# Kernel tuning notes

Measured on AMD Instinct MI355X. Metric: run time of the kernel, lower is better.

## Reference

```python
import jax, jax.numpy as jnp
import numpy as np

DIM = 128
NUM_HEADS = 8


def setup_inputs() -> dict:
    key = jax.random.key(0)
    ks = jax.random.split(key, 5)
    B, L, C = 4, 16384, DIM
    x = jax.random.normal(ks[0], (B, L, C), dtype=jnp.float32)
    # Linear params (stored as (in, out) so y = x @ W + b)
    w_qkv = jax.random.normal(ks[1], (C, 3 * C), dtype=jnp.float32) * (C ** -0.5)
    b_qkv = jax.random.normal(ks[2], (3 * C,), dtype=jnp.float32) * 0.02
    w_proj = jax.random.normal(ks[3], (C, C), dtype=jnp.float32) * (C ** -0.5)
    b_proj = jax.random.normal(ks[4], (C,), dtype=jnp.float32) * 0.02
    return {"x": x, "w_qkv": w_qkv, "b_qkv": b_qkv, "w_proj": w_proj, "b_proj": b_proj}


def reference(x, w_qkv, b_qkv, w_proj, b_proj):
    B, L, C = x.shape
    H = NUM_HEADS
    hd = C // H
    scale = C ** -0.5  # note: torch code scales by dim**-0.5, not head_dim**-0.5

    qkv = x @ w_qkv + b_qkv                      # (B, L, 3C)
    q, k, v = jnp.split(qkv, 3, axis=-1)         # each (B, L, C)

    def to_heads(t):
        return t.reshape(B, L, H, hd).transpose(0, 2, 1, 3)  # (B, H, L, hd)

    q, k, v = to_heads(q), to_heads(k), to_heads(v)

    # Per-token outer product over head_dim: (B, H, L, hd, hd)
    attn = (q * scale)[..., :, None] * k[..., None, :]
    attn = jax.nn.softmax(attn, axis=-1)

    # attn @ v per token: (B, H, L, hd)
    out = jnp.einsum("bhlij,bhlj->bhli", attn, v)
    out = out.transpose(0, 2, 1, 3).reshape(B, L, C)  # (B, L, C)
    return out @ w_proj + b_proj
```

## Files before the change

### kernel.cpp

```cpp
#include <hip/hip_runtime.h>


typedef __attribute__((ext_vector_type(8))) short bf16x8;
typedef __attribute__((ext_vector_type(4))) float f32x4;
typedef __attribute__((ext_vector_type(4))) unsigned int u32x4;

#define TILE_M 32
#define HALF_M 16
#define QKV_STRIDE_F 388
#define O_STRIDE 136

__device__ __forceinline__ unsigned short f2bf(float f) {
    unsigned int u = __builtin_bit_cast(unsigned int, f);
    u += 0x8000u;
    return (unsigned short)(u >> 16);
}
__device__ __forceinline__ unsigned int pkbf(float lo, float hi) {
    unsigned int a = __builtin_bit_cast(unsigned int, lo) + 0x8000u;
    unsigned int b = __builtin_bit_cast(unsigned int, hi) + 0x8000u;
    return __builtin_amdgcn_perm(b, a, 0x07060302u);
}

__global__ void prep_weights(const float* __restrict__ wqkv,
                             const float* __restrict__ wproj,
                             unsigned short* __restrict__ wqkvT,
                             unsigned short* __restrict__ wprojT) {
    int idx = blockIdx.x * 256 + threadIdx.x;
    if (idx < 384 * 128) {
        int n = idx >> 7, k = idx & 127;
        wqkvT[idx] = f2bf(wqkv[k * 384 + n]);
    }
    if (idx < 128 * 128) {
        int n = idx >> 7, k = idx & 127;
        wprojT[idx] = f2bf(wproj[k * 128 + n]);
    }
}

__global__ __launch_bounds__(256, 4) void fused_channel_attn(
    const float* __restrict__ x,
    const unsigned short* __restrict__ wqkvT,
    const float* __restrict__ bqkv,
    const unsigned short* __restrict__ wprojT,
    const float* __restrict__ bproj,
    float* __restrict__ out)
{
    __shared__ __align__(16) float us_f[HALF_M * QKV_STRIDE_F];
    __shared__ __align__(16) unsigned short us_o[TILE_M * O_STRIDE];

    const int tid  = threadIdx.x;
    const int lane = tid & 63;
    const int wave = tid >> 6;
    const int col  = lane & 15;
    const int quad = lane >> 4;
    const long base_tok = (long)blockIdx.x * TILE_M;

    int ntile[6];
    ntile[0] = 2 * wave;      ntile[1] = 2 * wave + 1;
    ntile[2] = 8 + 2 * wave;  ntile[3] = 9 + 2 * wave;
    ntile[4] = 16 + 2 * wave; ntile[5] = 17 + 2 * wave;

    bf16x8 afr[2][4];
#pragma unroll
    for (int m = 0; m < 2; ++m) {
        const float* xrow = x + (base_tok + m * 16 + col) * 128;
#pragma unroll
        for (int ks = 0; ks < 4; ++ks) {
            const float4* p = (const float4*)(xrow + ks * 32 + quad * 8);
            float4 f0 = p[0], f1 = p[1];
            u32x4 a = {pkbf(f0.x, f0.y), pkbf(f0.z, f0.w),
                       pkbf(f1.x, f1.y), pkbf(f1.z, f1.w)};
            afr[m][ks] = __builtin_bit_cast(bf16x8, a);
        }
    }

    f32x4 acc[2][6];
#pragma unroll
    for (int j = 0; j < 6; ++j) {
        float b = bqkv[ntile[j] * 16 + col];
        acc[0][j] = (f32x4){b, b, b, b};
        acc[1][j] = (f32x4){b, b, b, b};
    }
#pragma unroll
    for (int ks = 0; ks < 4; ++ks) {
        bf16x8 bfr[6];
#pragma unroll
        for (int j = 0; j < 6; ++j)
            bfr[j] = *(const bf16x8*)&wqkvT[(ntile[j] * 16 + col) * 128 + ks * 32 + quad * 8];
#pragma unroll
        for (int j = 0; j < 6; ++j) {
            acc[0][j] = __builtin_amdgcn_mfma_f32_16x16x32_bf16(afr[0][ks], bfr[j], acc[0][j], 0, 0, 0);
            acc[1][j] = __builtin_amdgcn_mfma_f32_16x16x32_bf16(afr[1][ks], bfr[j], acc[1][j], 0, 0, 0);
        }
    }

    const int t    = lane & 15;
    const int hbit = (lane >> 4) & 1;
    const int ih   = lane >> 5;
    const int h    = 2 * wave + hbit;
    const float* qkvrow = us_f + t * QKV_STRIDE_F + h * 16;
    const float sl2e = 0.08838834764831845f * 1.44269504088896340f;

    auto write_half = [&](int m) {
#pragma unroll
        for (int j = 0; j < 6; ++j)
#pragma unroll
            for (int r = 0; r < 4; ++r)
                us_f[(quad * 4 + r) * QKV_STRIDE_F + ntile[j] * 16 + col] = acc[m][j][r];
    };

    float4 kv4[4], vv4[4];
    auto read_half = [&]() {
#pragma unroll
        for (int c = 0; c < 4; ++c) {
            kv4[c] = ((const float4*)(qkvrow + 128))[c];
            vv4[c] = ((const float4*)(qkvrow + 256))[c];
        }
    };

    auto attn_half = [&](int mhalf) {
        unsigned short* orow = &us_o[(mhalf * 16 + t) * O_STRIDE + h * 16 + ih * 8];
        const float* qptr = qkvrow + ih * 8;
#pragma unroll 1
        for (int ip = 0; ip < 4; ++ip) {
            float q0 = qptr[ip * 2];
            float q1 = qptr[ip * 2 + 1];
            float ov0, ov1;
#pragma unroll
            for (int u = 0; u < 2; ++u) {
                float qs = (u ? q1 : q0) * sl2e;
                float den = 0.f, num = 0.f;
#pragma unroll
                for (int c = 0; c < 4; ++c) {
                    float e;
                    e = __builtin_amdgcn_exp2f(qs * kv4[c].x); den += e; num = fmaf(e, vv4[c].x, num);
                    e = __builtin_amdgcn_exp2f(qs * kv4[c].y); den += e; num = fmaf(e, vv4[c].y, num);
                    e = __builtin_amdgcn_exp2f(qs * kv4[c].z); den += e; num = fmaf(e, vv4[c].z, num);
                    e = __builtin_amdgcn_exp2f(qs * kv4[c].w); den += e; num = fmaf(e, vv4[c].w, num);
                }
                float o = num * __builtin_amdgcn_rcpf(den);
                if (u) ov1 = o; else ov0 = o;
            }
            *(unsigned int*)((char*)orow + ip * 4) = pkbf(ov0, ov1);
        }
    };

    write_half(0);
    read_half();
    attn_half(0);
    write_half(1);
    read_half();
    attn_half(1);

    __syncthreads();

    const int nb2 = wave * 2;
#pragma unroll
    for (int m = 0; m < 2; ++m) {
        bf16x8 af[4];
#pragma unroll
        for (int ks = 0; ks < 4; ++ks)
            af[ks] = *(const bf16x8*)&us_o[(m * 16 + col) * O_STRIDE + ks * 32 + quad * 8];
        f32x4 acc2[2];
#pragma unroll
        for (int n = 0; n < 2; ++n) {
            float b = bproj[(nb2 + n) * 16 + col];
            acc2[n] = (f32x4){b, b, b, b};
        }
#pragma unroll
        for (int ks = 0; ks < 4; ++ks) {
            bf16x8 bb[2];
#pragma unroll
            for (int n = 0; n < 2; ++n)
                bb[n] = *(const bf16x8*)&wprojT[((nb2 + n) * 16 + col) * 128 + ks * 32 + quad * 8];
#pragma unroll
            for (int n = 0; n < 2; ++n)
                acc2[n] = __builtin_amdgcn_mfma_f32_16x16x32_bf16(af[ks], bb[n], acc2[n], 0, 0, 0);
        }
#pragma unroll
        for (int n = 0; n < 2; ++n)
#pragma unroll
            for (int r = 0; r < 4; ++r) {
                long tt = base_tok + m * 16 + quad * 4 + r;
                out[tt * 128 + (nb2 + n) * 16 + col] = acc2[n][r];
            }
    }
}

extern "C" void kernel_launch(void* const* d_in, const int* in_sizes, int n_in,
                              void* d_out, int out_size, void* d_ws, size_t ws_size,
                              hipStream_t stream) {
    const float* x     = (const float*)d_in[0];
    const float* wqkv  = (const float*)d_in[1];
    const float* bqkv  = (const float*)d_in[2];
    const float* wproj = (const float*)d_in[3];
    const float* bproj = (const float*)d_in[4];
    float* out = (float*)d_out;

    unsigned short* wqkvT  = (unsigned short*)d_ws;
    unsigned short* wprojT = wqkvT + 384 * 128;

    prep_weights<<<192, 256, 0, stream>>>(wqkv, wproj, wqkvT, wprojT);

    const int tokens = in_sizes[0] / 128;
    fused_channel_attn<<<tokens / TILE_M, 256, 0, stream>>>(
        x, wqkvT, bqkv, wprojT, bproj, out);
}
```

Baseline: 131.9 us.

## Swap MFMA operands to keep QKV in registers and use lane shuffles

The QKV GEMM now puts the weight fragment in the A slot, so each lane's accumulator holds four head-dim elements of a single token. The per-token outer-product softmax then gathers that token's K and V values with xor-shuffles across lanes instead of staging the full QKV tile through shared memory. This removes the large fp32 LDS buffer along with its write and read traffic, which should also allow more resident blocks. The cost is 24 cross-lane shuffles per stage and more live registers in the unrolled softmax loops.

```diff
diff --git a/kernel.cpp b/kernel.cpp
--- a/kernel.cpp
+++ b/kernel.cpp
@@ -4,10 +4,9 @@
 typedef __attribute__((ext_vector_type(8))) short bf16x8;
 typedef __attribute__((ext_vector_type(4))) float f32x4;
 typedef __attribute__((ext_vector_type(4))) unsigned int u32x4;
+typedef __attribute__((ext_vector_type(2))) unsigned int u32x2;
 
 #define TILE_M 32
-#define HALF_M 16
-#define QKV_STRIDE_F 388
 #define O_STRIDE 136
 
 __device__ __forceinline__ unsigned short f2bf(float f) {
@@ -20,6 +19,8 @@
     unsigned int b = __builtin_bit_cast(unsigned int, hi) + 0x8000u;
     return __builtin_amdgcn_perm(b, a, 0x07060302u);
 }
+__device__ __forceinline__ float sx16(float v) { return __shfl_xor(v, 16, 64); }
+__device__ __forceinline__ float sx32(float v) { return __shfl_xor(v, 32, 64); }
 
 __global__ void prep_weights(const float* __restrict__ wqkv,
                              const float* __restrict__ wproj,
@@ -44,7 +45,6 @@
     const float* __restrict__ bproj,
     float* __restrict__ out)
 {
-    __shared__ __align__(16) float us_f[HALF_M * QKV_STRIDE_F];
     __shared__ __align__(16) unsigned short us_o[TILE_M * O_STRIDE];
 
     const int tid  = threadIdx.x;
@@ -76,9 +76,9 @@
     f32x4 acc[2][6];
 #pragma unroll
     for (int j = 0; j < 6; ++j) {
-        float b = bqkv[ntile[j] * 16 + col];
-        acc[0][j] = (f32x4){b, b, b, b};
-        acc[1][j] = (f32x4){b, b, b, b};
+        f32x4 b4 = *(const f32x4*)&bqkv[ntile[j] * 16 + quad * 4];
+        acc[0][j] = b4;
+        acc[1][j] = b4;
     }
 #pragma unroll
     for (int ks = 0; ks < 4; ++ks) {
@@ -88,68 +88,59 @@
             bfr[j] = *(const bf16x8*)&wqkvT[(ntile[j] * 16 + col) * 128 + ks * 32 + quad * 8];
 #pragma unroll
         for (int j = 0; j < 6; ++j) {
-            acc[0][j] = __builtin_amdgcn_mfma_f32_16x16x32_bf16(afr[0][ks], bfr[j], acc[0][j], 0, 0, 0);
-            acc[1][j] = __builtin_amdgcn_mfma_f32_16x16x32_bf16(afr[1][ks], bfr[j], acc[1][j], 0, 0, 0);
+            acc[0][j] = __builtin_amdgcn_mfma_f32_16x16x32_bf16(bfr[j], afr[0][ks], acc[0][j], 0, 0, 0);
+            acc[1][j] = __builtin_amdgcn_mfma_f32_16x16x32_bf16(bfr[j], afr[1][ks], acc[1][j], 0, 0, 0);
         }
     }
 
-    const int t    = lane & 15;
-    const int hbit = (lane >> 4) & 1;
-    const int ih   = lane >> 5;
-    const int h    = 2 * wave + hbit;
-    const float* qkvrow = us_f + t * QKV_STRIDE_F + h * 16;
     const float sl2e = 0.08838834764831845f * 1.44269504088896340f;
 
-    auto write_half = [&](int m) {
-#pragma unroll
-        for (int j = 0; j < 6; ++j)
-#pragma unroll
-            for (int r = 0; r < 4; ++r)
-                us_f[(quad * 4 + r) * QKV_STRIDE_F + ntile[j] * 16 + col] = acc[m][j][r];
-    };
+#define STAGE_B(MM, HB)                                                        \
+    do {                                                                       \
+        f32x4 qq = acc[MM][HB];                                                \
+        f32x4 kq = acc[MM][2 + HB];                                            \
+        f32x4 vq = acc[MM][4 + HB];                                            \
+        float ka0 = kq[0], ka1 = kq[1], ka2 = kq[2], ka3 = kq[3];              \
+        float va0 = vq[0], va1 = vq[1], va2 = vq[2], va3 = vq[3];              \
+        float ka4 = sx16(ka0), ka5 = sx16(ka1), ka6 = sx16(ka2), ka7 = sx16(ka3); \
+        float va4 = sx16(va0), va5 = sx16(va1), va6 = sx16(va2), va7 = sx16(va3); \
+        float kb0 = sx32(ka0), kb1 = sx32(ka1), kb2 = sx32(ka2), kb3 = sx32(ka3); \
+        float kb4 = sx32(ka4), kb5 = sx32(ka5), kb6 = sx32(ka6), kb7 = sx32(ka7); \
+        float vb0 = sx32(va0), vb1 = sx32(va1), vb2 = sx32(va2), vb3 = sx32(va3); \
+        float vb4 = sx32(va4), vb5 = sx32(va5), vb6 = sx32(va6), vb7 = sx32(va7); \
+        float ov[4];                                                           \
+        _Pragma("unroll")                                                      \
+        for (int i = 0; i < 4; ++i) {                                          \
+            float qs = qq[i] * sl2e;                                           \
+            float den = 0.f, num = 0.f, e;                                     \
+            e = __builtin_amdgcn_exp2f(qs * ka0); den += e; num = fmaf(e, va0, num); \
+            e = __builtin_amdgcn_exp2f(qs * ka1); den += e; num = fmaf(e, va1, num); \
+            e = __builtin_amdgcn_exp2f(qs * ka2); den += e; num = fmaf(e, va2, num); \
+            e = __builtin_amdgcn_exp2f(qs * ka3); den += e; num = fmaf(e, va3, num); \
+            e = __builtin_amdgcn_exp2f(qs * ka4); den += e; num = fmaf(e, va4, num); \
+            e = __builtin_amdgcn_exp2f(qs * ka5); den += e; num = fmaf(e, va5, num); \
+            e = __builtin_amdgcn_exp2f(qs * ka6); den += e; num = fmaf(e, va6, num); \
+            e = __builtin_amdgcn_exp2f(qs * ka7); den += e; num = fmaf(e, va7, num); \
+            e = __builtin_amdgcn_exp2f(qs * kb0); den += e; num = fmaf(e, vb0, num); \
+            e = __builtin_amdgcn_exp2f(qs * kb1); den += e; num = fmaf(e, vb1, num); \
+            e = __builtin_amdgcn_exp2f(qs * kb2); den += e; num = fmaf(e, vb2, num); \
+            e = __builtin_amdgcn_exp2f(qs * kb3); den += e; num = fmaf(e, vb3, num); \
+            e = __builtin_amdgcn_exp2f(qs * kb4); den += e; num = fmaf(e, vb4, num); \
+            e = __builtin_amdgcn_exp2f(qs * kb5); den += e; num = fmaf(e, vb5, num); \
+            e = __builtin_amdgcn_exp2f(qs * kb6); den += e; num = fmaf(e, vb6, num); \
+            e = __builtin_amdgcn_exp2f(qs * kb7); den += e; num = fmaf(e, vb7, num); \
+            ov[i] = num * __builtin_amdgcn_rcpf(den);                          \
+        }                                                                      \
+        u32x2 op = {pkbf(ov[0], ov[1]), pkbf(ov[2], ov[3])};                   \
+        *(u32x2*)&us_o[((MM) * 16 + col) * O_STRIDE +                          \
+                       (2 * wave + (HB)) * 16 + quad * 4] = op;                \
+    } while (0)
 
-    float4 kv4[4], vv4[4];
-    auto read_half = [&]() {
-#pragma unroll
-        for (int c = 0; c < 4; ++c) {
-            kv4[c] = ((const float4*)(qkvrow + 128))[c];
-            vv4[c] = ((const float4*)(qkvrow + 256))[c];
-        }
-    };
-
-    auto attn_half = [&](int mhalf) {
-        unsigned short* orow = &us_o[(mhalf * 16 + t) * O_STRIDE + h * 16 + ih * 8];
-        const float* qptr = qkvrow + ih * 8;
-#pragma unroll 1
-        for (int ip = 0; ip < 4; ++ip) {
-            float q0 = qptr[ip * 2];
-            float q1 = qptr[ip * 2 + 1];
-            float ov0, ov1;
-#pragma unroll
-            for (int u = 0; u < 2; ++u) {
-                float qs = (u ? q1 : q0) * sl2e;
-                float den = 0.f, num = 0.f;
-#pragma unroll
-                for (int c = 0; c < 4; ++c) {
-                    float e;
-                    e = __builtin_amdgcn_exp2f(qs * kv4[c].x); den += e; num = fmaf(e, vv4[c].x, num);
-                    e = __builtin_amdgcn_exp2f(qs * kv4[c].y); den += e; num = fmaf(e, vv4[c].y, num);
-                    e = __builtin_amdgcn_exp2f(qs * kv4[c].z); den += e; num = fmaf(e, vv4[c].z, num);
-                    e = __builtin_amdgcn_exp2f(qs * kv4[c].w); den += e; num = fmaf(e, vv4[c].w, num);
-                }
-                float o = num * __builtin_amdgcn_rcpf(den);
-                if (u) ov1 = o; else ov0 = o;
-            }
-            *(unsigned int*)((char*)orow + ip * 4) = pkbf(ov0, ov1);
-        }
-    };
-
-    write_half(0);
-    read_half();
-    attn_half(0);
-    write_half(1);
-    read_half();
-    attn_half(1);
+    STAGE_B(0, 0);
+    STAGE_B(0, 1);
+    STAGE_B(1, 0);
+    STAGE_B(1, 1);
+#undef STAGE_B
 
     __syncthreads();
 
```

After: 138.3 us. 4.9% more time.
